# Kernel optimization log

Hardware: AMD Instinct MI355X
Metric: run time of the kernel (lower is better)

## Reference

```python
import jax, jax.numpy as jnp
import numpy as np

# Config constants (MLAConfig)
B, S = 1, 2048                 # batch, context_len (prefill: seq == context_len)
H = 16                         # num_heads
DN, DR, DV = 128, 64, 128      # qk_nope_head_dim, qk_rope_head_dim, v_head_dim
QL, C = 1536, 512              # q_lora_rank, kv_lora_rank
BLK = 128                      # fp8 dequant block size
MAX_CACHE = 4096
SOFTMAX_SCALE = 1.0 / np.sqrt(DN + DR)  # 1/sqrt(192)
NEG_INF = -10000.0


def gen_rope(n_total, head_size):
    # theta_j = 10000^{-2j/d}; idx_theta[i, 0, :] = [i*theta, i*theta] (repeated halves)
    theta = 1.0 / (10000.0 ** (jnp.arange(0, head_size, 2, dtype=jnp.float32) / head_size))
    idx = jnp.outer(jnp.arange(n_total, dtype=jnp.float32), theta)  # (N, d/2)
    return jnp.tile(idx[:, None, :], (1, 1, 2))                     # (N, 1, d)


def fp8_dequant(x, s, block=BLK):
    # Block-wise dequant: x (M,N) * per-(block x block) scale s (M/b, N/b).
    M, N = x.shape
    m, n = M // block, N // block  # shapes chosen divisible by block -> no padding
    return (x.reshape(m, block, n, block) * s[:, None, :, None]).reshape(M, N)


def apply_rope(x, cos, sin):
    # x: (B*S, heads, d). Interleaved RoPE: de-interleave pairs into halves,
    # then x*cos + rotate_half(x)*sin with cos/sin (B*S, 1, d).
    bs, h, d = x.shape
    x = x.reshape(bs, h, d // 2, 2).transpose(0, 1, 3, 2).reshape(bs, h, d)
    rot = jnp.concatenate([-x[..., d // 2:], x[..., :d // 2]], axis=-1)
    return x * cos + rot * sin


def setup_inputs() -> dict:
    key = jax.random.key(0)
    ks = jax.random.split(key, 9)
    WUQ = jax.random.normal(ks[0], (H * (DN + DR), QL), dtype=jnp.float32)
    WUKV = jax.random.normal(ks[1], (H * (DN + DV), C), dtype=jnp.float32)
    # positive, small block scales so attention logits stay well-conditioned
    WUQ_scale = 0.05 * jax.random.uniform(ks[2], (H * (DN + DR) // BLK, QL // BLK), dtype=jnp.float32)
    WUKV_scale = 0.05 * jax.random.uniform(ks[3], (H * (DN + DV) // BLK, C // BLK), dtype=jnp.float32)
    Q = jax.random.normal(ks[4], (B, S, QL), dtype=jnp.float32)
    KV = jax.random.normal(ks[5], (B, S, C), dtype=jnp.float32)
    PE = jax.random.normal(ks[6], (B, S, DR), dtype=jnp.float32)
    kv_cache = jax.random.normal(ks[7], (B, MAX_CACHE, C), dtype=jnp.float32)
    pe_cache = jax.random.normal(ks[8], (B, MAX_CACHE, DR), dtype=jnp.float32)
    idx_theta = gen_rope(B * S, DR)
    mask = jnp.triu(jnp.full((S, S), NEG_INF, dtype=jnp.float32), k=1)
    return {"WUQ": WUQ, "WUQ_scale": WUQ_scale, "WUKV": WUKV, "WUKV_scale": WUKV_scale,
            "Q": Q, "KV": KV, "PE": PE, "kv_cache": kv_cache, "pe_cache": pe_cache,
            "idx_theta": idx_theta, "mask": mask}


def reference(WUQ, WUQ_scale, WUKV, WUKV_scale, Q, KV, PE, kv_cache, pe_cache, idx_theta, mask):
    bsz, seqlen, _ = Q.shape
    # fp8 block-wise dequant of the low-rank up-projection weights
    WUQd = fp8_dequant(WUQ, WUQ_scale)
    WUKVd = fp8_dequant(WUKV, WUKV_scale)
    # Q up-projection from q_lora latent: (B*S, QL) @ (QL, H*(DN+DR))
    q = (Q.reshape(-1, QL) @ WUQd.T).reshape(bsz, seqlen, H, DN + DR)
    q_nope, q_pe = q[..., :DN], q[..., DN:]
    cos, sin = jnp.cos(idx_theta), jnp.sin(idx_theta)  # (B*S, 1, DR)
    q_pe = apply_rope(q_pe.reshape(bsz * seqlen, H, DR), cos, sin).reshape(bsz, seqlen, H, DR)
    k_pe = apply_rope(PE.reshape(bsz * seqlen, 1, DR), cos, sin).reshape(bsz, seqlen, DR)
    # absorbed low-rank K matrix: q_nope projected into the kv latent space
    W3 = WUKVd.reshape(H, DN + DV, C)
    q_lat = jnp.einsum('bshd,hdc->bshc', q_nope, W3[:, :DN])
    # continuous-cache prefill: write fresh latents into the cache, attend over them
    kv = kv_cache.at[:, :seqlen].set(KV)[:, :seqlen]   # (B, S, C)
    pe = pe_cache.at[:, :seqlen].set(k_pe)[:, :seqlen]  # (B, S, DR)
    scores = (jnp.einsum('bshc,btc->bsht', q_lat, kv)
              + jnp.einsum('bshr,btr->bsht', q_pe, pe)) * SOFTMAX_SCALE
    scores = scores + mask[None, :, None, :]
    attn = jax.nn.softmax(scores, axis=-1)
    x = jnp.einsum('bsht,btc->bshc', attn, kv)
    out = jnp.einsum('bshc,hdc->bshd', x, W3[:, DN:])  # V up-projection (absorbed)
    return out  # (B, S, H, DV)
```

## Files before the change

kernel.cpp:

```cpp
#include <hip/hip_runtime.h>

typedef __bf16 bf16_t;
typedef __attribute__((ext_vector_type(4))) __bf16 bf16x4;
typedef __attribute__((ext_vector_type(8))) __bf16 bf16x8;
typedef __attribute__((ext_vector_type(4))) float f32x4;

#define SOFTMAX_SCALE 0.07216878364870322f
#define NEG_MASK (-10000.0f)

__device__ __forceinline__ void async16(const bf16_t* g, bf16_t* l) {
  __builtin_amdgcn_global_load_lds(
      (const __attribute__((address_space(1))) unsigned int*)g,
      (__attribute__((address_space(3))) unsigned int*)l, 16, 0, 0);
}


__global__ void k_dequant(const float* __restrict__ W, const float* __restrict__ S,
                          bf16_t* __restrict__ out, int cols, int scols) {
  int i = (blockIdx.x * 256 + threadIdx.x) * 4;
  int r = i / cols, c = i % cols;
  float s = S[(r >> 7) * scols + (c >> 7)];
  float4 w = *(const float4*)(W + i);
  out[i + 0] = (bf16_t)(w.x * s);
  out[i + 1] = (bf16_t)(w.y * s);
  out[i + 2] = (bf16_t)(w.z * s);
  out[i + 3] = (bf16_t)(w.w * s);
}

__global__ void k_f32_to_bf16(const float* __restrict__ in, bf16_t* __restrict__ out) {
  int i = (blockIdx.x * 256 + threadIdx.x) * 4;
  float4 v = *(const float4*)(in + i);
  out[i + 0] = (bf16_t)(v.x * SOFTMAX_SCALE);
  out[i + 1] = (bf16_t)(v.y * SOFTMAX_SCALE);
  out[i + 2] = (bf16_t)(v.z * SOFTMAX_SCALE);
  out[i + 3] = (bf16_t)(v.w * SOFTMAX_SCALE);
}

__global__ void k_wv1t(const bf16_t* __restrict__ Wd, bf16_t* __restrict__ Wt) {
  __shared__ bf16_t Lt[64][72];
  int h = blockIdx.x >> 4;
  int d0 = ((blockIdx.x >> 3) & 1) * 64;
  int c0 = (blockIdx.x & 7) * 64;
  int t = threadIdx.x;
#pragma unroll
  for (int j = 0; j < 2; ++j) {
    int ch = t * 2 + j, r = ch >> 3, c8 = ch & 7;
    bf16x8 v = *(const bf16x8*)(Wd + (size_t)(h * 256 + d0 + r) * 512 + c0 + c8 * 8);
    *(bf16x8*)&Lt[r][c8 * 8] = v;
  }
  __syncthreads();
#pragma unroll
  for (int j = 0; j < 2; ++j) {
    int ch = t * 2 + j, cc = ch >> 3, dd8 = ch & 7;
    bf16x8 o;
#pragma unroll
    for (int e = 0; e < 8; ++e) o[e] = Lt[dd8 * 8 + e][cc];
    *(bf16x8*)(Wt + (size_t)h * 65536 + (c0 + cc) * 128 + d0 + dd8 * 8) = o;
  }
}

__global__ void k_k4(const float* __restrict__ KV, bf16_t* __restrict__ K4) {
  int i = blockIdx.x * 256 + threadIdx.x;
  int c2 = i & 15, t = i >> 4;
  int tt = t >> 6, k = t & 63;
  const float* src = KV + (size_t)t * 512 + c2 * 32;
  bf16_t* dst = K4 + (size_t)tt * 36864 + c2 * 2048 + k * 8;
#pragma unroll
  for (int sub = 0; sub < 4; ++sub) {
    float4 u = *(const float4*)(src + sub * 8);
    float4 v = *(const float4*)(src + sub * 8 + 4);
    bf16x8 o;
    o[0] = (bf16_t)u.x; o[1] = (bf16_t)u.y; o[2] = (bf16_t)u.z; o[3] = (bf16_t)u.w;
    o[4] = (bf16_t)v.x; o[5] = (bf16_t)v.y; o[6] = (bf16_t)v.z; o[7] = (bf16_t)v.w;
    *(bf16x8*)(dst + sub * 512) = o;
  }
}

__global__ void k_v4(const float* __restrict__ KV, bf16_t* __restrict__ V4) {
  int i = blockIdx.x * 256 + threadIdx.x;
  int c = i & 511, a = i >> 9;
  int t0 = a * 8, tt = t0 >> 6;
  int key0 = t0 & 63, kk2 = key0 >> 5, sub = (key0 >> 3) & 3;
  bf16x8 o;
#pragma unroll
  for (int j = 0; j < 8; ++j)
    o[j] = (bf16_t)KV[(size_t)(t0 + j) * 512 + c];
  *(bf16x8*)(V4 + (size_t)tt * 32768 + kk2 * 16384 + sub * 4096 + c * 8) = o;
}

__global__ void k_pe_rope(const float* __restrict__ PE, const float* __restrict__ idxt,
                          bf16_t* __restrict__ K4) {
  int i = blockIdx.x * 256 + threadIdx.x;
  int t = i >> 5, j = i & 31;
  float a = idxt[t * 64 + j];
  float c1 = cosf(a), s1 = sinf(a);
  float e = PE[t * 64 + 2 * j], o = PE[t * 64 + 2 * j + 1];
  int tt = t >> 6, k = t & 63;
  bf16_t* base = K4 + (size_t)tt * 36864 + (j >> 3) * 512 + k * 8 + (j & 7);
  base[16 * 2048] = (bf16_t)(e * c1 - o * s1);
  base[17 * 2048] = (bf16_t)(o * c1 + e * s1);
}

__global__ void k_q_rope(const bf16_t* __restrict__ q, const float* __restrict__ idxt,
                         bf16_t* __restrict__ qfull) {
  int i = blockIdx.x * 256 + threadIdx.x;
  int j = i & 31, h = (i >> 5) & 15, t = i >> 9;
  float a = idxt[t * 64 + j];
  float c1 = cosf(a), s1 = sinf(a);
  const bf16_t* src = q + t * 3072 + h * 192 + 128;
  float e = (float)src[2 * j], o = (float)src[2 * j + 1];
  bf16_t* dst = qfull + (size_t)h * 2048 * 576 + t * 576 + 512;
  dst[j]      = (bf16_t)(e * c1 - o * s1);
  dst[32 + j] = (bf16_t)(o * c1 + e * s1);
}

template <int OUT_F32>
__global__ __launch_bounds__(256) void k_gemm3(
    const bf16_t* __restrict__ A, int lda, long saz,
    const bf16_t* __restrict__ B, int ldb, long sbz,
    void* __restrict__ Cv, int ldc, long scz, int K) {
  __shared__ __attribute__((aligned(16))) bf16_t At[2][8192];
  __shared__ __attribute__((aligned(16))) bf16_t Bt[2][8192];
  const int tid = threadIdx.x;
  const int lane = tid & 63;
  const int wv = tid >> 6;
  const int fr = lane & 15, fq = lane >> 4;
  const int wm = (wv & 1) * 64, wn = (wv >> 1) * 64;
  const int m0 = blockIdx.x * 128, n0 = blockIdx.y * 128;
  const bf16_t* Ab = A + (long)blockIdx.z * saz;
  const bf16_t* Bb = B + (long)blockIdx.z * sbz;

#define STAGE3(bufp, ks)                                                    \
  do {                                                                      \
    _Pragma("unroll") for (int i_ = 0; i_ < 4; ++i_) {                      \
      int ch_ = tid + i_ * 256;                                             \
      int ar_ = ch_ >> 3;                                                   \
      int c8_ = (ch_ & 7) ^ (ar_ & 7);                                      \
      async16(Ab + (size_t)(m0 + ar_) * lda + (ks) * 64 + c8_ * 8,          \
              At[bufp] + ch_ * 8);                                          \
      async16(Bb + (size_t)(n0 + ar_) * ldb + (ks) * 64 + c8_ * 8,          \
              Bt[bufp] + ch_ * 8);                                          \
    }                                                                       \
  } while (0)

  f32x4 acc[4][4] = {};
  const int nks = K >> 6;
  STAGE3(0, 0);
  for (int ks = 0; ks < nks; ++ks) {
    int buf = ks & 1;
    __syncthreads();
    if (ks + 1 < nks) STAGE3(buf ^ 1, ks + 1);
#pragma unroll
    for (int kkl = 0; kkl < 2; ++kkl) {
      bf16x8 af[4], bfr[4];
#pragma unroll
      for (int m = 0; m < 4; ++m) {
        int row = wm + m * 16 + fr;
        af[m] = *(const bf16x8*)(At[buf] + (row * 8 + (((kkl * 4 + fq) ^ (row & 7)))) * 8);
      }
#pragma unroll
      for (int n = 0; n < 4; ++n) {
        int row = wn + n * 16 + fr;
        bfr[n] = *(const bf16x8*)(Bt[buf] + (row * 8 + (((kkl * 4 + fq) ^ (row & 7)))) * 8);
      }
#pragma unroll
      for (int m = 0; m < 4; ++m)
#pragma unroll
        for (int n = 0; n < 4; ++n)
          acc[m][n] = __builtin_amdgcn_mfma_f32_16x16x32_bf16(af[m], bfr[n], acc[m][n], 0, 0, 0);
    }
  }
#undef STAGE3
#pragma unroll
  for (int m = 0; m < 4; ++m) {
    int row = m0 + wm + m * 16 + fq * 4;
#pragma unroll
    for (int n = 0; n < 4; ++n) {
      int col = n0 + wn + n * 16 + fr;
#pragma unroll
      for (int i = 0; i < 4; ++i) {
        if (OUT_F32)
          ((float*)Cv)[(long)blockIdx.z * scz + (size_t)(row + i) * ldc + col] = acc[m][n][i];
        else
          ((bf16_t*)Cv)[(long)blockIdx.z * scz + (size_t)(row + i) * ldc + col] = (bf16_t)acc[m][n][i];
      }
    }
  }
}

__global__ __attribute__((amdgpu_flat_work_group_size(512, 512),
                          amdgpu_waves_per_eu(2, 2)))
void k_attn(const bf16_t* __restrict__ qfull,
            const bf16_t* __restrict__ K4,
            const bf16_t* __restrict__ V4,
            bf16_t* __restrict__ X) {
  __shared__ __attribute__((aligned(16))) bf16_t Kt[18 * 2048];
  __shared__ __attribute__((aligned(16))) bf16_t Vt[2 * 16384];
  __shared__ __attribute__((aligned(16))) bf16_t P[64 * 64];
  __shared__ __attribute__((aligned(16))) bf16_t Qpe[8 * 512];
  __shared__ float lred[4][64];

  const int tid = threadIdx.x;
  const int lane = tid & 63;
  const int w = tid >> 6;
  const int fr = lane & 15, fq = lane >> 4;
  const int h = blockIdx.x & 15;
  const int qt = 31 - (blockIdx.x >> 4);
  const int nt = qt + 1;
  const int rg = w >> 2;
  const int kq = w & 3;

  const bf16_t* qh = qfull + (size_t)h * 2048 * 576;
  bf16_t* Xh = X + (size_t)h * 2048 * 512;

  {
    int row = tid >> 3, sub = tid & 7;
    bf16x8 v = *(const bf16x8*)(qh + (size_t)(qt * 64 + row) * 576 + 512 + sub * 8);
    *(bf16x8*)(Qpe + sub * 512 + row * 8) = v;
  }

  bf16x8 qa[2][16];
  {
    const bf16_t* qb = qh + (size_t)(qt * 64 + rg * 32) * 576;
#pragma unroll
    for (int mf = 0; mf < 2; ++mf)
#pragma unroll
      for (int kk = 0; kk < 16; ++kk)
        qa[mf][kk] = *(const bf16x8*)(qb + (mf * 16 + fr) * 576 + kk * 32 + fq * 8);
  }

#pragma unroll
  for (int i = 0; i < 9; ++i) {
    int ck = w + 8 * i;
    async16(K4 + ck * 512 + lane * 8, Kt + ck * 512 + lane * 8);
  }

  f32x4 acc[2][8] = {};
  float lreg[2] = {0.f, 0.f};

  for (int t = 0; t < nt; ++t) {
    __syncthreads();

    {
      const bf16_t* vsrc = V4 + (size_t)t * 32768;
#pragma unroll
      for (int i = 0; i < 8; ++i) {
        int cv = w + 8 * i;
        async16(vsrc + cv * 512 + lane * 8, Vt + cv * 512 + lane * 8);
      }
    }

    f32x4 sA[2] = {}, sB[2] = {};
    __builtin_amdgcn_s_setprio(1);
#pragma unroll
    for (int kk = 0; kk < 16; kk += 2) {
      bf16x8 kf0 = *(const bf16x8*)(Kt + kk * 2048 + fq * 512 + (kq * 16 + fr) * 8);
      bf16x8 kf1 = *(const bf16x8*)(Kt + (kk + 1) * 2048 + fq * 512 + (kq * 16 + fr) * 8);
      sA[0] = __builtin_amdgcn_mfma_f32_16x16x32_bf16(kf0, qa[0][kk], sA[0], 0, 0, 0);
      sA[1] = __builtin_amdgcn_mfma_f32_16x16x32_bf16(kf0, qa[1][kk], sA[1], 0, 0, 0);
      sB[0] = __builtin_amdgcn_mfma_f32_16x16x32_bf16(kf1, qa[0][kk + 1], sB[0], 0, 0, 0);
      sB[1] = __builtin_amdgcn_mfma_f32_16x16x32_bf16(kf1, qa[1][kk + 1], sB[1], 0, 0, 0);
    }
    {
      bf16x8 kf0 = *(const bf16x8*)(Kt + 16 * 2048 + fq * 512 + (kq * 16 + fr) * 8);
      bf16x8 kf1 = *(const bf16x8*)(Kt + 17 * 2048 + fq * 512 + (kq * 16 + fr) * 8);
      bf16x8 q00 = *(const bf16x8*)(Qpe + fq * 512 + (rg * 32 + fr) * 8);
      bf16x8 q01 = *(const bf16x8*)(Qpe + fq * 512 + (rg * 32 + 16 + fr) * 8);
      bf16x8 q10 = *(const bf16x8*)(Qpe + (4 + fq) * 512 + (rg * 32 + fr) * 8);
      bf16x8 q11 = *(const bf16x8*)(Qpe + (4 + fq) * 512 + (rg * 32 + 16 + fr) * 8);
      sA[0] = __builtin_amdgcn_mfma_f32_16x16x32_bf16(kf0, q00, sA[0], 0, 0, 0);
      sA[1] = __builtin_amdgcn_mfma_f32_16x16x32_bf16(kf0, q01, sA[1], 0, 0, 0);
      sB[0] = __builtin_amdgcn_mfma_f32_16x16x32_bf16(kf1, q10, sB[0], 0, 0, 0);
      sB[1] = __builtin_amdgcn_mfma_f32_16x16x32_bf16(kf1, q11, sB[1], 0, 0, 0);
    }
    __builtin_amdgcn_s_setprio(0);
    f32x4 s[2];
#pragma unroll
    for (int mf = 0; mf < 2; ++mf)
#pragma unroll
      for (int i = 0; i < 4; ++i) s[mf][i] = sA[mf][i] + sB[mf][i];

    bool diag = (t == qt);
#pragma unroll
    for (int mf = 0; mf < 2; ++mf) {
      int qrow = rg * 32 + mf * 16 + fr;
      if (diag) {
#pragma unroll
        for (int i = 0; i < 4; ++i) {
          int kcol = kq * 16 + fq * 4 + i;
          if (kcol > qrow) s[mf][i] += NEG_MASK;
        }
      }
      float p0 = __expf(s[mf][0]);
      float p1 = __expf(s[mf][1]);
      float p2 = __expf(s[mf][2]);
      float p3 = __expf(s[mf][3]);
      bf16x4 pk;
      pk[0] = (bf16_t)p0; pk[1] = (bf16_t)p1; pk[2] = (bf16_t)p2; pk[3] = (bf16_t)p3;
      int chunk = (kq * 2 + (fq >> 1)) ^ (qrow & 7);
      *(bf16x4*)(P + qrow * 64 + chunk * 8 + (fq & 1) * 4) = pk;
      lreg[mf] += (p0 + p1) + (p2 + p3);
    }
    __syncthreads();

    if (t + 1 < nt) {
      const bf16_t* ksrc = K4 + (size_t)(t + 1) * 36864;
#pragma unroll
      for (int i = 0; i < 9; ++i) {
        int ck = w + 8 * i;
        async16(ksrc + ck * 512 + lane * 8, Kt + ck * 512 + lane * 8);
      }
    }

    __builtin_amdgcn_s_setprio(1);
#pragma unroll
    for (int kk2 = 0; kk2 < 2; ++kk2) {
      bf16x8 pa[2];
#pragma unroll
      for (int mf = 0; mf < 2; ++mf) {
        int qrow = rg * 32 + mf * 16 + fr;
        pa[mf] = *(const bf16x8*)(P + qrow * 64 + (((kk2 * 4 + fq) ^ (qrow & 7)) * 8));
      }
#pragma unroll
      for (int nf = 0; nf < 8; ++nf) {
        bf16x8 vb = *(const bf16x8*)(Vt + kk2 * 16384 + fq * 4096 + (kq * 128 + nf * 16 + fr) * 8);
        acc[0][nf] = __builtin_amdgcn_mfma_f32_16x16x32_bf16(pa[0], vb, acc[0][nf], 0, 0, 0);
        acc[1][nf] = __builtin_amdgcn_mfma_f32_16x16x32_bf16(pa[1], vb, acc[1][nf], 0, 0, 0);
      }
    }
    __builtin_amdgcn_s_setprio(0);
  }

#pragma unroll
  for (int mf = 0; mf < 2; ++mf) {
    float lw = lreg[mf];
    lw += __shfl_xor(lw, 16);
    lw += __shfl_xor(lw, 32);
    if (fq == 0) lred[kq][rg * 32 + mf * 16 + fr] = lw;
  }
  __syncthreads();

  {
    bf16_t* XT = Kt;
#pragma unroll
    for (int mf = 0; mf < 2; ++mf)
#pragma unroll
      for (int i = 0; i < 4; ++i) {
        int row = rg * 32 + mf * 16 + fq * 4 + i;
        float invl = 1.0f / ((lred[0][row] + lred[1][row]) + (lred[2][row] + lred[3][row]));
#pragma unroll
        for (int nf = 0; nf < 8; ++nf)
          XT[row * 512 + kq * 128 + nf * 16 + fr] = (bf16_t)(acc[mf][nf][i] * invl);
      }
  }
  __syncthreads();
#pragma unroll
  for (int it = 0; it < 8; ++it) {
    int id = tid + it * 512;
    int row = id >> 6, j = id & 63;
    *(bf16x8*)(Xh + (size_t)(qt * 64 + row) * 512 + j * 8) = *(const bf16x8*)(Kt + row * 512 + j * 8);
  }
}


extern "C" void kernel_launch(void* const* d_in, const int* in_sizes, int n_in,
                              void* d_out, int out_size, void* d_ws, size_t ws_size,
                              hipStream_t stream) {
  (void)in_sizes; (void)n_in; (void)out_size; (void)ws_size;
  const float* WUQ   = (const float*)d_in[0];
  const float* WUQs  = (const float*)d_in[1];
  const float* WUKV  = (const float*)d_in[2];
  const float* WUKVs = (const float*)d_in[3];
  const float* Q     = (const float*)d_in[4];
  const float* KV    = (const float*)d_in[5];
  const float* PE    = (const float*)d_in[6];
  const float* idxt  = (const float*)d_in[9];
  float* out = (float*)d_out;

  char* ws = (char*)d_ws;
  size_t off = 0;
  auto alloc = [&](size_t n) -> char* {
    char* p = ws + off;
    off += (n + 255) & ~(size_t)255;
    return p;
  };
  bf16_t* WUQd  = (bf16_t*)alloc((size_t)3072 * 1536 * 2);
  bf16_t* Qb    = (bf16_t*)alloc((size_t)2048 * 1536 * 2);
  bf16_t* WUKVd = (bf16_t*)alloc((size_t)4096 * 512 * 2);
  bf16_t* Wv1t  = (bf16_t*)alloc((size_t)16 * 512 * 128 * 2);
  bf16_t* qbuf  = (bf16_t*)alloc((size_t)2048 * 3072 * 2);
  bf16_t* K4    = (bf16_t*)alloc((size_t)32 * 36864 * 2);
  bf16_t* V4    = (bf16_t*)alloc((size_t)32 * 32768 * 2);
  bf16_t* qfull = (bf16_t*)alloc((size_t)16 * 2048 * 576 * 2);
  bf16_t* Xb    = (bf16_t*)alloc((size_t)16 * 2048 * 512 * 2);

  k_dequant<<<4608, 256, 0, stream>>>(WUQ, WUQs, WUQd, 1536, 12);
  k_dequant<<<2048, 256, 0, stream>>>(WUKV, WUKVs, WUKVd, 512, 4);
  k_f32_to_bf16<<<3072, 256, 0, stream>>>(Q, Qb);
  k_wv1t<<<256, 256, 0, stream>>>(WUKVd, Wv1t);
  k_k4<<<128, 256, 0, stream>>>(KV, K4);
  k_v4<<<512, 256, 0, stream>>>(KV, V4);
  k_pe_rope<<<256, 256, 0, stream>>>(PE, idxt, K4);
  k_gemm3<0><<<dim3(16, 24, 1), 256, 0, stream>>>(Qb, 1536, 0, WUQd, 1536, 0,
                                                  qbuf, 3072, 0, 1536);
  k_q_rope<<<4096, 256, 0, stream>>>(qbuf, idxt, qfull);
  k_gemm3<0><<<dim3(16, 4, 16), 256, 0, stream>>>(qbuf, 3072, 192, Wv1t, 128, (long)512 * 128,
                                                  qfull, 576, (long)2048 * 576, 128);
  k_attn<<<dim3(512), dim3(512), 0, stream>>>(qfull, K4, V4, Xb);
  k_gemm3<1><<<dim3(16, 1, 16), 256, 0, stream>>>(Xb, 512, (long)2048 * 512,
                                                  WUKVd + 128 * 512, 512, (long)256 * 512,
                                                  out, 2048, 128, 512);
}
```

Before: 203.7 us.

## Merge preprocessing kernels into one launch and fuse q RoPE into GEMM epilogue

Seven preprocessing kernels (weight dequant, Q cast, K/V relayout, PE RoPE, Wv1t transpose) become one kernel that branches on block index. The transpose now reads fp32 weights and dequantizes them directly, and only the V half of WUKV is dequantized to bf16. The q RoPE step moves into the epilogue of the first GEMM using a lane shuffle, which removes one separate kernel and a reread of qbuf. The goal is fewer launches and less memory traffic, at the cost of branch divergence and extra cos/sin work inside the GEMM epilogue.

```diff
diff --git a/kernel.cpp b/kernel.cpp
--- a/kernel.cpp
+++ b/kernel.cpp
@@ -14,111 +14,119 @@
       (__attribute__((address_space(3))) unsigned int*)l, 16, 0, 0);
 }
 
-
-__global__ void k_dequant(const float* __restrict__ W, const float* __restrict__ S,
-                          bf16_t* __restrict__ out, int cols, int scols) {
-  int i = (blockIdx.x * 256 + threadIdx.x) * 4;
-  int r = i / cols, c = i % cols;
-  float s = S[(r >> 7) * scols + (c >> 7)];
-  float4 w = *(const float4*)(W + i);
-  out[i + 0] = (bf16_t)(w.x * s);
-  out[i + 1] = (bf16_t)(w.y * s);
-  out[i + 2] = (bf16_t)(w.z * s);
-  out[i + 3] = (bf16_t)(w.w * s);
+__global__ void k_prep(const float* __restrict__ WUQ, const float* __restrict__ WUQs,
+                       bf16_t* __restrict__ WUQd,
+                       const float* __restrict__ WUKV, const float* __restrict__ WUKVs,
+                       bf16_t* __restrict__ WUKVd, bf16_t* __restrict__ Wv1t,
+                       const float* __restrict__ Q, bf16_t* __restrict__ Qb,
+                       const float* __restrict__ KV, bf16_t* __restrict__ K4,
+                       bf16_t* __restrict__ V4,
+                       const float* __restrict__ PE, const float* __restrict__ idxt) {
+  __shared__ bf16_t Lt[64][72];
+  const int b = blockIdx.x;
+  const int tid = threadIdx.x;
+
+  if (b < 4608) {
+    int i = (b * 256 + tid) * 4;
+    int r = i / 1536, c = i % 1536;
+    float s = WUQs[(r >> 7) * 12 + (c >> 7)];
+    float4 w = *(const float4*)(WUQ + i);
+    WUQd[i + 0] = (bf16_t)(w.x * s);
+    WUQd[i + 1] = (bf16_t)(w.y * s);
+    WUQd[i + 2] = (bf16_t)(w.z * s);
+    WUQd[i + 3] = (bf16_t)(w.w * s);
+  } else if (b < 5632) {
+    int i4 = ((b - 4608) * 256 + tid) * 4;
+    int h = i4 >> 16, within = i4 & 65535;
+    int row = 128 + (within >> 9), col = within & 511;
+    int R = h * 256 + row;
+    float s = WUKVs[(R >> 7) * 4 + (col >> 7)];
+    const float* src = WUKV + (size_t)R * 512 + col;
+    float4 w = *(const float4*)src;
+    bf16_t* dst = WUKVd + (size_t)R * 512 + col;
+    dst[0] = (bf16_t)(w.x * s);
+    dst[1] = (bf16_t)(w.y * s);
+    dst[2] = (bf16_t)(w.z * s);
+    dst[3] = (bf16_t)(w.w * s);
+  } else if (b < 8704) {
+    int i = ((b - 5632) * 256 + tid) * 4;
+    float4 v = *(const float4*)(Q + i);
+    Qb[i + 0] = (bf16_t)(v.x * SOFTMAX_SCALE);
+    Qb[i + 1] = (bf16_t)(v.y * SOFTMAX_SCALE);
+    Qb[i + 2] = (bf16_t)(v.z * SOFTMAX_SCALE);
+    Qb[i + 3] = (bf16_t)(v.w * SOFTMAX_SCALE);
+  } else if (b < 8832) {
+    int i = (b - 8704) * 256 + tid;
+    int c2 = i & 15, t = i >> 4;
+    int tt = t >> 6, k = t & 63;
+    const float* src = KV + (size_t)t * 512 + c2 * 32;
+    bf16_t* dst = K4 + (size_t)tt * 36864 + c2 * 2048 + k * 8;
+#pragma unroll
+    for (int sub = 0; sub < 4; ++sub) {
+      float4 u = *(const float4*)(src + sub * 8);
+      float4 v = *(const float4*)(src + sub * 8 + 4);
+      bf16x8 o;
+      o[0] = (bf16_t)u.x; o[1] = (bf16_t)u.y; o[2] = (bf16_t)u.z; o[3] = (bf16_t)u.w;
+      o[4] = (bf16_t)v.x; o[5] = (bf16_t)v.y; o[6] = (bf16_t)v.z; o[7] = (bf16_t)v.w;
+      *(bf16x8*)(dst + sub * 512) = o;
+    }
+  } else if (b < 9344) {
+    int i = (b - 8832) * 256 + tid;
+    int c = i & 511, a = i >> 9;
+    int t0 = a * 8, tt = t0 >> 6;
+    int key0 = t0 & 63, kk2 = key0 >> 5, sub = (key0 >> 3) & 3;
+    bf16x8 o;
+#pragma unroll
+    for (int j = 0; j < 8; ++j)
+      o[j] = (bf16_t)KV[(size_t)(t0 + j) * 512 + c];
+    *(bf16x8*)(V4 + (size_t)tt * 32768 + kk2 * 16384 + sub * 4096 + c * 8) = o;
+  } else if (b < 9600) {
+    int i = (b - 9344) * 256 + tid;
+    int t = i >> 5, j = i & 31;
+    float a = idxt[t * 64 + j];
+    float c1 = cosf(a), s1 = sinf(a);
+    float e = PE[t * 64 + 2 * j], o = PE[t * 64 + 2 * j + 1];
+    int tt = t >> 6, k = t & 63;
+    bf16_t* base = K4 + (size_t)tt * 36864 + (j >> 3) * 512 + k * 8 + (j & 7);
+    base[16 * 2048] = (bf16_t)(e * c1 - o * s1);
+    base[17 * 2048] = (bf16_t)(o * c1 + e * s1);
+  } else {
+    int bb = b - 9600;
+    int h = bb >> 4;
+    int d0 = ((bb >> 3) & 1) * 64;
+    int c0 = (bb & 7) * 64;
+    float s = WUKVs[8 * h + (c0 >> 7)];
+#pragma unroll
+    for (int j = 0; j < 2; ++j) {
+      int ch = tid * 2 + j, r = ch >> 3, c8 = ch & 7;
+      const float* src = WUKV + (size_t)(h * 256 + d0 + r) * 512 + c0 + c8 * 8;
+      float4 u = *(const float4*)src;
+      float4 v = *(const float4*)(src + 4);
+      bf16x8 o;
+      o[0] = (bf16_t)(u.x * s); o[1] = (bf16_t)(u.y * s);
+      o[2] = (bf16_t)(u.z * s); o[3] = (bf16_t)(u.w * s);
+      o[4] = (bf16_t)(v.x * s); o[5] = (bf16_t)(v.y * s);
+      o[6] = (bf16_t)(v.z * s); o[7] = (bf16_t)(v.w * s);
+      *(bf16x8*)&Lt[r][c8 * 8] = o;
+    }
+    __syncthreads();
+#pragma unroll
+    for (int j = 0; j < 2; ++j) {
+      int ch = tid * 2 + j, cc = ch >> 3, dd8 = ch & 7;
+      bf16x8 o;
+#pragma unroll
+      for (int e = 0; e < 8; ++e) o[e] = Lt[dd8 * 8 + e][cc];
+      *(bf16x8*)(Wv1t + (size_t)h * 65536 + (c0 + cc) * 128 + d0 + dd8 * 8) = o;
+    }
+  }
 }
 
-__global__ void k_f32_to_bf16(const float* __restrict__ in, bf16_t* __restrict__ out) {
-  int i = (blockIdx.x * 256 + threadIdx.x) * 4;
-  float4 v = *(const float4*)(in + i);
-  out[i + 0] = (bf16_t)(v.x * SOFTMAX_SCALE);
-  out[i + 1] = (bf16_t)(v.y * SOFTMAX_SCALE);
-  out[i + 2] = (bf16_t)(v.z * SOFTMAX_SCALE);
-  out[i + 3] = (bf16_t)(v.w * SOFTMAX_SCALE);
-}
-
-__global__ void k_wv1t(const bf16_t* __restrict__ Wd, bf16_t* __restrict__ Wt) {
-  __shared__ bf16_t Lt[64][72];
-  int h = blockIdx.x >> 4;
-  int d0 = ((blockIdx.x >> 3) & 1) * 64;
-  int c0 = (blockIdx.x & 7) * 64;
-  int t = threadIdx.x;
-#pragma unroll
-  for (int j = 0; j < 2; ++j) {
-    int ch = t * 2 + j, r = ch >> 3, c8 = ch & 7;
-    bf16x8 v = *(const bf16x8*)(Wd + (size_t)(h * 256 + d0 + r) * 512 + c0 + c8 * 8);
-    *(bf16x8*)&Lt[r][c8 * 8] = v;
-  }
-  __syncthreads();
-#pragma unroll
-  for (int j = 0; j < 2; ++j) {
-    int ch = t * 2 + j, cc = ch >> 3, dd8 = ch & 7;
-    bf16x8 o;
-#pragma unroll
-    for (int e = 0; e < 8; ++e) o[e] = Lt[dd8 * 8 + e][cc];
-    *(bf16x8*)(Wt + (size_t)h * 65536 + (c0 + cc) * 128 + d0 + dd8 * 8) = o;
-  }
-}
-
-__global__ void k_k4(const float* __restrict__ KV, bf16_t* __restrict__ K4) {
-  int i = blockIdx.x * 256 + threadIdx.x;
-  int c2 = i & 15, t = i >> 4;
-  int tt = t >> 6, k = t & 63;
-  const float* src = KV + (size_t)t * 512 + c2 * 32;
-  bf16_t* dst = K4 + (size_t)tt * 36864 + c2 * 2048 + k * 8;
-#pragma unroll
-  for (int sub = 0; sub < 4; ++sub) {
-    float4 u = *(const float4*)(src + sub * 8);
-    float4 v = *(const float4*)(src + sub * 8 + 4);
-    bf16x8 o;
-    o[0] = (bf16_t)u.x; o[1] = (bf16_t)u.y; o[2] = (bf16_t)u.z; o[3] = (bf16_t)u.w;
-    o[4] = (bf16_t)v.x; o[5] = (bf16_t)v.y; o[6] = (bf16_t)v.z; o[7] = (bf16_t)v.w;
-    *(bf16x8*)(dst + sub * 512) = o;
-  }
-}
-
-__global__ void k_v4(const float* __restrict__ KV, bf16_t* __restrict__ V4) {
-  int i = blockIdx.x * 256 + threadIdx.x;
-  int c = i & 511, a = i >> 9;
-  int t0 = a * 8, tt = t0 >> 6;
-  int key0 = t0 & 63, kk2 = key0 >> 5, sub = (key0 >> 3) & 3;
-  bf16x8 o;
-#pragma unroll
-  for (int j = 0; j < 8; ++j)
-    o[j] = (bf16_t)KV[(size_t)(t0 + j) * 512 + c];
-  *(bf16x8*)(V4 + (size_t)tt * 32768 + kk2 * 16384 + sub * 4096 + c * 8) = o;
-}
-
-__global__ void k_pe_rope(const float* __restrict__ PE, const float* __restrict__ idxt,
-                          bf16_t* __restrict__ K4) {
-  int i = blockIdx.x * 256 + threadIdx.x;
-  int t = i >> 5, j = i & 31;
-  float a = idxt[t * 64 + j];
-  float c1 = cosf(a), s1 = sinf(a);
-  float e = PE[t * 64 + 2 * j], o = PE[t * 64 + 2 * j + 1];
-  int tt = t >> 6, k = t & 63;
-  bf16_t* base = K4 + (size_t)tt * 36864 + (j >> 3) * 512 + k * 8 + (j & 7);
-  base[16 * 2048] = (bf16_t)(e * c1 - o * s1);
-  base[17 * 2048] = (bf16_t)(o * c1 + e * s1);
-}
-
-__global__ void k_q_rope(const bf16_t* __restrict__ q, const float* __restrict__ idxt,
-                         bf16_t* __restrict__ qfull) {
-  int i = blockIdx.x * 256 + threadIdx.x;
-  int j = i & 31, h = (i >> 5) & 15, t = i >> 9;
-  float a = idxt[t * 64 + j];
-  float c1 = cosf(a), s1 = sinf(a);
-  const bf16_t* src = q + t * 3072 + h * 192 + 128;
-  float e = (float)src[2 * j], o = (float)src[2 * j + 1];
-  bf16_t* dst = qfull + (size_t)h * 2048 * 576 + t * 576 + 512;
-  dst[j]      = (bf16_t)(e * c1 - o * s1);
-  dst[32 + j] = (bf16_t)(o * c1 + e * s1);
-}
-
-template <int OUT_F32>
+template <int MODE>
 __global__ __launch_bounds__(256) void k_gemm3(
     const bf16_t* __restrict__ A, int lda, long saz,
     const bf16_t* __restrict__ B, int ldb, long sbz,
-    void* __restrict__ Cv, int ldc, long scz, int K) {
+    void* __restrict__ Cv, int ldc, long scz, int K,
+    const float* __restrict__ idxt, bf16_t* __restrict__ qfull) {
   __shared__ __attribute__((aligned(16))) bf16_t At[2][8192];
   __shared__ __attribute__((aligned(16))) bf16_t Bt[2][8192];
   const int tid = threadIdx.x;
@@ -173,16 +181,36 @@
 #undef STAGE3
 #pragma unroll
   for (int m = 0; m < 4; ++m) {
-    int row = m0 + wm + m * 16 + fq * 4;
+    int row0 = m0 + wm + m * 16 + fq * 4;
 #pragma unroll
     for (int n = 0; n < 4; ++n) {
       int col = n0 + wn + n * 16 + fr;
 #pragma unroll
       for (int i = 0; i < 4; ++i) {
-        if (OUT_F32)
-          ((float*)Cv)[(long)blockIdx.z * scz + (size_t)(row + i) * ldc + col] = acc[m][n][i];
+        if (MODE == 1)
+          ((float*)Cv)[(long)blockIdx.z * scz + (size_t)(row0 + i) * ldc + col] = acc[m][n][i];
         else
-          ((bf16_t*)Cv)[(long)blockIdx.z * scz + (size_t)(row + i) * ldc + col] = (bf16_t)acc[m][n][i];
+          ((bf16_t*)Cv)[(long)blockIdx.z * scz + (size_t)(row0 + i) * ldc + col] = (bf16_t)acc[m][n][i];
+      }
+      if (MODE == 2) {
+        int head = col / 192;
+        int within = col % 192;
+        bool pe = within >= 128;
+        int j = (within - 128) >> 1;
+        bool evenc = (within & 1) == 0;
+#pragma unroll
+        for (int i = 0; i < 4; ++i) {
+          int row = row0 + i;
+          float v = acc[m][n][i];
+          float other = __shfl_xor(v, 1);
+          if (pe) {
+            float a = idxt[row * 64 + j];
+            float c1 = cosf(a), s1 = sinf(a);
+            bf16_t* dst = qfull + (size_t)head * 2048 * 576 + (size_t)row * 576 + 512;
+            if (evenc) dst[j]      = (bf16_t)(v * c1 - other * s1);
+            else       dst[32 + j] = (bf16_t)(v * c1 + other * s1);
+          }
+        }
       }
     }
   }
@@ -394,20 +422,15 @@
   bf16_t* qfull = (bf16_t*)alloc((size_t)16 * 2048 * 576 * 2);
   bf16_t* Xb    = (bf16_t*)alloc((size_t)16 * 2048 * 512 * 2);
 
-  k_dequant<<<4608, 256, 0, stream>>>(WUQ, WUQs, WUQd, 1536, 12);
-  k_dequant<<<2048, 256, 0, stream>>>(WUKV, WUKVs, WUKVd, 512, 4);
-  k_f32_to_bf16<<<3072, 256, 0, stream>>>(Q, Qb);
-  k_wv1t<<<256, 256, 0, stream>>>(WUKVd, Wv1t);
-  k_k4<<<128, 256, 0, stream>>>(KV, K4);
-  k_v4<<<512, 256, 0, stream>>>(KV, V4);
-  k_pe_rope<<<256, 256, 0, stream>>>(PE, idxt, K4);
-  k_gemm3<0><<<dim3(16, 24, 1), 256, 0, stream>>>(Qb, 1536, 0, WUQd, 1536, 0,
-                                                  qbuf, 3072, 0, 1536);
-  k_q_rope<<<4096, 256, 0, stream>>>(qbuf, idxt, qfull);
+  k_prep<<<9856, 256, 0, stream>>>(WUQ, WUQs, WUQd, WUKV, WUKVs, WUKVd, Wv1t,
+                                   Q, Qb, KV, K4, V4, PE, idxt);
+  k_gemm3<2><<<dim3(16, 24, 1), 256, 0, stream>>>(Qb, 1536, 0, WUQd, 1536, 0,
+                                                  qbuf, 3072, 0, 1536, idxt, qfull);
   k_gemm3<0><<<dim3(16, 4, 16), 256, 0, stream>>>(qbuf, 3072, 192, Wv1t, 128, (long)512 * 128,
-                                                  qfull, 576, (long)2048 * 576, 128);
+                                                  qfull, 576, (long)2048 * 576, 128,
+                                                  nullptr, nullptr);
   k_attn<<<dim3(512), dim3(512), 0, stream>>>(qfull, K4, V4, Xb);
   k_gemm3<1><<<dim3(16, 1, 16), 256, 0, stream>>>(Xb, 512, (long)2048 * 512,
                                                   WUKVd + 128 * 512, 512, (long)256 * 512,
-                                                  out, 2048, 128, 512);
+                                                  out, 2048, 128, 512, nullptr, nullptr);
 }
```

Result: slower. 458.6 us (+125.1%).
